# Kernel tuning notes

Hardware: AMD Instinct MI355X
Metric: run time of the kernel (lower is better)

## Reference

```python
import jax, jax.numpy as jnp
import numpy as np

DIM = 24
HID = 256
N = 4096
NUM_LO = DIM * (DIM - 1) // 2  # 276
NEG = -0.01  # slope used in the hand-written Jacobians (source uses -0.01, NOT the fwd leaky slope 0.01; faithful)


def _linear_params(key, out_dim, in_dim):
    kw, kb = jax.random.split(key)
    s = 1.0 / np.sqrt(in_dim)
    W = jax.random.uniform(kw, (out_dim, in_dim), jnp.float32, -s, s)
    b = jax.random.uniform(kb, (out_dim,), jnp.float32, -s, s)
    return W, b


def setup_inputs() -> dict:
    key = jax.random.key(0)
    k = jax.random.split(key, 7)
    W1, b1 = _linear_params(k[0], HID, DIM)
    W2, b2 = _linear_params(k[1], HID, HID)
    WG, bG = _linear_params(k[2], DIM, HID)
    WLd, bLd = _linear_params(k[3], DIM, HID)
    WLo, bLo = _linear_params(k[4], NUM_LO, HID)
    q = jax.random.normal(k[5], (N, DIM), jnp.float32)
    q_dot = jax.random.normal(k[6], (N, DIM), jnp.float32)
    return {"q": q, "q_dot": q_dot, "W1": W1, "b1": b1, "W2": W2, "b2": b2,
            "WG": WG, "bG": bG, "WLd": WLd, "bLd": bLd, "WLo": WLo, "bLo": bLo}


def _forward(q, q_dot, W1, b1, W2, b2, WG, bG, WLd, bLd, WLo, bLo):
    n, d = q.shape
    tr, tc = np.tril_indices(d, -1)  # row-major strict-lower order == torch mask-flatten order
    di = np.arange(d)
    # MLP trunk (torch leaky_relu default slope 0.01)
    h1 = jax.nn.leaky_relu(q @ W1.T + b1)                       # [n,HID]
    h2 = jax.nn.leaky_relu(h1 @ W2.T + b2)                      # [n,HID]
    h3 = h2 @ WLd.T + bLd                                       # [n,d]
    g = h2 @ WG.T + bG                                          # [n,d]
    Ld = jax.nn.softplus(h3)                                    # [n,d]
    Lo = h2 @ WLo.T + bLo                                       # [n,NUM_LO]
    # Lower-triangular L (diag_embed(Ld) + masked strict-lower fill)
    L = jnp.zeros((n, d, d), q.dtype).at[:, tr, tc].set(Lo).at[:, di, di].set(Ld)
    # Hand-written Jacobian chain; diag_embed(v)@W == v[:,:,None]*W (direct elementwise scaling)
    dR1 = jnp.where(h1 > 0, 1.0, NEG)
    J1 = dR1[:, :, None] * W1                                    # dh1/dq  [n,HID,d]
    dR2 = jnp.where(h2 > 0, 1.0, NEG)
    J2 = dR2[:, :, None] * jnp.einsum('ij,njd->nid', W2, J1)     # dh2/dq  [n,HID,d]
    sig = jax.nn.sigmoid(h3)
    dld_dq = sig[:, :, None] * jnp.einsum('ij,njd->nid', WLd, J2)  # [n,d,d]
    dlo_dq = jnp.einsum('oj,njd->nod', WLo, J2)                  # [n,NUM_LO,d]
    dld_dt = jnp.einsum('nid,nd->ni', dld_dq, q_dot)             # [n,d]
    dlo_dt = jnp.einsum('nod,nd->no', dlo_dq, q_dot)             # [n,NUM_LO]
    dL_dt = jnp.zeros((n, d, d), q.dtype).at[:, tr, tc].set(dlo_dt).at[:, di, di].set(dld_dt)
    # 4D assembly: torch does L[L==1] = dlo_dq.view(-1), which reinterprets the (lo, q_idx)
    # flat buffer in (q_idx, tril_pos) order -> plain reshape replicates that exactly.
    vals = dlo_dq.reshape(n, d, NUM_LO)
    dld_dq_p = dld_dq.transpose(0, 2, 1)                         # [n, d_q, d_ld]
    dL_dq = jnp.zeros((n, d, d, d), q.dtype).at[:, :, tr, tc].set(vals).at[:, :, di, di].set(dld_dq_p)
    eye = jnp.eye(d, dtype=q.dtype)
    M = L @ L.transpose(0, 2, 1) + 1e-9 * eye
    dM_dt = L @ dL_dt.transpose(0, 2, 1) + dL_dt @ L.transpose(0, 2, 1)
    # Quadratic term. torch: q_dot.repeat(d,1)/L.repeat(d,1,1) index as (i % n) while
    # dL_dq.view(n*d,d,d) indexes as (i // d, i % d) -> replicate exactly (faithful).
    idx = jnp.arange(n * d) % n
    qd_r = q_dot[idx]                                            # [n*d, d]
    L_r = L[idx]                                                 # [n*d, d, d]
    dL_i = dL_dq.reshape(n * d, d, d)
    S = dL_i @ L_r.transpose(0, 2, 1) + L_r @ dL_i.transpose(0, 2, 1)
    quad = jnp.einsum('bi,bij,bj->b', qd_r, S, qd_r).reshape(n, d)
    c = jnp.einsum('nij,nj->ni', dM_dt, q_dot) - 0.5 * quad
    return M, c, g


def reference(q, q_dot, W1, b1, W2, b2, WG, bG, WLd, bLd, WLo, bLo):
    return _forward(q, q_dot, W1, b1, W2, b2, WG, bG, WLd, bLd, WLo, bLo)
```

## Files before the change

### kernel.cpp

```cpp
#include <hip/hip_runtime.h>
#include <math.h>

#define DIM 24
#define HID 256
#define NLO 276
#define NSAMP 4096
#define C_OFF 2359296
#define G_OFF 2457600

#define OFF_W2FH 0
#define OFF_W2FL 32768
#define OFF_WEFH 65536
#define OFF_WEFL 106496
#define OFF_W1H16 147456
#define OFF_W1L16 151552
#define OFF_W2H16 155648
#define OFF_W2L16 188416
#define OFF_WHH16 221184
#define OFF_WHL16 264192
#define OFF_MSKT 307200
#define OFF_SIGT 372736
#define OFF_LDT  471040
#define OFF_UT   569344
#define OFF_LOT  667648

typedef __attribute__((ext_vector_type(8))) short bf16x8;
typedef __attribute__((ext_vector_type(8))) _Float16 f16x8;
typedef __attribute__((ext_vector_type(4))) float f32x4;

__device__ __forceinline__ float leaky(float x){ return x > 0.f ? x : 0.01f*x; }
__device__ __forceinline__ unsigned short f2b(float f){
  unsigned u = __float_as_uint(f);
  return (unsigned short)((u + 0x7FFFu + ((u >> 16) & 1u)) >> 16);
}
__device__ __forceinline__ float b2f(unsigned short h){ return __uint_as_float(((unsigned)h) << 16); }
__device__ __forceinline__ void f2h2(float v, unsigned short* hi, unsigned short* lo){
  _Float16 h = (_Float16)v;
  _Float16 l = (_Float16)((v - (float)h) * 4096.f);
  *hi = *(unsigned short*)&h; *lo = *(unsigned short*)&l;
}

__global__ __launch_bounds__(256) void k0_prep(
    const float* __restrict__ W1, const float* __restrict__ W2,
    const float* __restrict__ WG, const float* __restrict__ WLd,
    const float* __restrict__ WLo, float* __restrict__ ws)
{
  const int tid = blockIdx.x*256 + threadIdx.x;
  const int nth = gridDim.x*256;
  unsigned short* W2FH = (unsigned short*)(ws + OFF_W2FH);
  unsigned short* W2FL = (unsigned short*)(ws + OFF_W2FL);
  for (int e = tid; e < 65536; e += nth){
    int j=e&7, l=(e>>3)&63, kb=(e>>9)&7, mt=e>>12;
    int m = mt*16+(l&15), k = kb*32+((l>>4)&3)*8+j;
    float v = W2[m*256+k];
    unsigned short h = f2b(v);
    W2FH[e]=h; W2FL[e]=f2b(v-b2f(h));
  }
  unsigned short* WEFH = (unsigned short*)(ws + OFF_WEFH);
  unsigned short* WEFL = (unsigned short*)(ws + OFF_WEFL);
  for (int e = tid; e < 81920; e += nth){
    int j=e&7, l=(e>>3)&63, kb=(e>>9)&7, mt=e>>12;
    int r = mt*16+(l&15), k = kb*32+((l>>4)&3)*8+j;
    float v = 0.f;
    if (r < 24) v = WLd[r*256+k]; else if (r < 300) v = WLo[(r-24)*256+k];
    unsigned short h = f2b(v);
    WEFH[e]=h; WEFL[e]=f2b(v-b2f(h));
  }
  unsigned short* W1H = (unsigned short*)(ws + OFF_W1H16);
  unsigned short* W1L = (unsigned short*)(ws + OFF_W1L16);
  for (int e = tid; e < 8192; e += nth){
    int j=e&7, l=(e>>3)&63, mt=e>>9;
    int m = mt*16+(l&15), k = ((l>>4)&3)*8+j;
    float v = (k < 24) ? W1[m*24+k] : 0.f;
    f2h2(v, &W1H[e], &W1L[e]);
  }
  unsigned short* W2H = (unsigned short*)(ws + OFF_W2H16);
  unsigned short* W2L = (unsigned short*)(ws + OFF_W2L16);
  for (int e = tid; e < 65536; e += nth){
    int j=e&7, l=(e>>3)&63, kb=(e>>9)&7, mt=e>>12;
    int m = mt*16+(l&15), k = kb*32+((l>>4)&3)*8+j;
    f2h2(W2[m*256+k], &W2H[e], &W2L[e]);
  }
  unsigned short* WHH = (unsigned short*)(ws + OFF_WHH16);
  unsigned short* WHL = (unsigned short*)(ws + OFF_WHL16);
  for (int e = tid; e < 86016; e += nth){
    int j=e&7, l=(e>>3)&63, kb=(e>>9)&7, mt=e>>12;
    int rr = mt*16+(l&15), k = kb*32+((l>>4)&3)*8+j;
    float v = 0.f;
    if (rr < 24) v = WLd[rr*256+k];
    else if (rr < 48) v = WG[(rr-24)*256+k];
    else if (rr < 324) v = WLo[(rr-48)*256+k];
    f2h2(v, &WHH[e], &WHL[e]);
  }
}

__global__ __launch_bounds__(256) void k1_fwd(
    const float* __restrict__ q,
    const float* __restrict__ b1, const float* __restrict__ b2,
    const float* __restrict__ bG, const float* __restrict__ bLd,
    const float* __restrict__ bLo, float* __restrict__ ws,
    float* __restrict__ out)
{
  const int s0 = blockIdx.x*8, t = threadIdx.x;
  const int w = t>>6, l = t&63, l15 = l&15, l4g = (l>>4)&3;
  unsigned* MSKT = (unsigned*)(ws + OFF_MSKT);
  float* SIGT = ws + OFF_SIGT;
  float* LDT  = ws + OFF_LDT;
  float* LOT  = ws + OFF_LOT;

  __shared__ __align__(16) unsigned short pool[8448];
  __shared__ unsigned char mb[8][64];
  unsigned short* BQH = pool;
  unsigned short* BQL = BQH + 320;
  unsigned short* BH2 = pool;
  unsigned short* BL2 = BH2 + 2112;

  for (int f = t; f < 192; f += 256){
    float v = q[s0*24 + f];
    int n = f/24, k = f%24;
    f2h2(v, &BQH[n*40+k], &BQL[n*40+k]);
  }
  if (t < 64){ int n = t>>3, k = 24 + (t&7); BQH[n*40+k]=0; BQL[n*40+k]=0; }
  __syncthreads();

  f32x4 aH[4], aX[4];
  #pragma unroll
  for (int i=0;i<4;++i){ aH[i]=(f32x4){0,0,0,0}; aX[i]=(f32x4){0,0,0,0}; }
  {
    const f16x8* WH = (const f16x8*)(ws + OFF_W1H16);
    const f16x8* WL = (const f16x8*)(ws + OFF_W1L16);
    f16x8 Af[4], Al[4];
    #pragma unroll
    for (int i=0;i<4;++i){ int mt=w+4*i; Af[i]=WH[mt*64+l]; Al[i]=WL[mt*64+l]; }
    int off = l15*40 + l4g*8;
    f16x8 Bh = *(const f16x8*)(BQH+off), Bl = *(const f16x8*)(BQL+off);
    #pragma unroll
    for (int i=0;i<4;++i){
      aH[i]=__builtin_amdgcn_mfma_f32_16x16x32_f16(Af[i],Bh,aH[i],0,0,0);
      aX[i]=__builtin_amdgcn_mfma_f32_16x16x32_f16(Af[i],Bl,aX[i],0,0,0);
      aX[i]=__builtin_amdgcn_mfma_f32_16x16x32_f16(Al[i],Bh,aX[i],0,0,0);
    }
  }
  __syncthreads();
  #pragma unroll
  for (int i=0;i<4;++i){
    int m0=(w+4*i)*16+4*l4g;
    float4 bb = *(const float4*)(b1+m0);
    int n = l15;
    if (n < 8){
      unsigned nib=0; unsigned short hs[4], ls[4];
      #pragma unroll
      for (int r=0;r<4;++r){
        float val = aH[i][r] + aX[i][r]*(1.f/4096.f) + ((const float*)&bb)[r];
        if (val > 0.f) nib |= 1u<<r;
        f2h2(leaky(val), &hs[r], &ls[r]);
      }
      mb[n][(m0>>2)] = (unsigned char)nib;
      *(uint2*)(BH2 + n*264 + m0) = make_uint2((unsigned)hs[0]|((unsigned)hs[1]<<16),
                                               (unsigned)hs[2]|((unsigned)hs[3]<<16));
      *(uint2*)(BL2 + n*264 + m0) = make_uint2((unsigned)ls[0]|((unsigned)ls[1]<<16),
                                               (unsigned)ls[2]|((unsigned)ls[3]<<16));
    }
  }
  __syncthreads();
  if (t < 64){
    int n = t&7, w8 = t>>3; unsigned word = 0;
    #pragma unroll
    for (int b=0;b<8;++b) word |= (unsigned)(mb[n][w8*8+b] & 0xFu) << (4*b);
    MSKT[w8*NSAMP + s0+n] = word;
  }

  #pragma unroll
  for (int i=0;i<4;++i){ aH[i]=(f32x4){0,0,0,0}; aX[i]=(f32x4){0,0,0,0}; }
  {
    const f16x8* WH = (const f16x8*)(ws + OFF_W2H16);
    const f16x8* WL = (const f16x8*)(ws + OFF_W2L16);
    for (int kb=0;kb<8;++kb){
      f16x8 Af[4], Al[4];
      #pragma unroll
      for (int i=0;i<4;++i){ int mt=w+4*i; Af[i]=WH[(mt*8+kb)*64+l]; Al[i]=WL[(mt*8+kb)*64+l]; }
      int off = l15*264 + kb*32 + l4g*8;
      f16x8 Bh = *(const f16x8*)(BH2+off), Bl = *(const f16x8*)(BL2+off);
      #pragma unroll
      for (int i=0;i<4;++i){
        aH[i]=__builtin_amdgcn_mfma_f32_16x16x32_f16(Af[i],Bh,aH[i],0,0,0);
        aX[i]=__builtin_amdgcn_mfma_f32_16x16x32_f16(Af[i],Bl,aX[i],0,0,0);
        aX[i]=__builtin_amdgcn_mfma_f32_16x16x32_f16(Al[i],Bh,aX[i],0,0,0);
      }
    }
  }
  __syncthreads();
  #pragma unroll
  for (int i=0;i<4;++i){
    int m0=(w+4*i)*16+4*l4g;
    float4 bb = *(const float4*)(b2+m0);
    int n = l15;
    if (n < 8){
      unsigned nib=0; unsigned short hs[4], ls[4];
      #pragma unroll
      for (int r=0;r<4;++r){
        float val = aH[i][r] + aX[i][r]*(1.f/4096.f) + ((const float*)&bb)[r];
        if (val > 0.f) nib |= 1u<<r;
        f2h2(leaky(val), &hs[r], &ls[r]);
      }
      mb[n][(m0>>2)] = (unsigned char)nib;
      *(uint2*)(BH2 + n*264 + m0) = make_uint2((unsigned)hs[0]|((unsigned)hs[1]<<16),
                                               (unsigned)hs[2]|((unsigned)hs[3]<<16));
      *(uint2*)(BL2 + n*264 + m0) = make_uint2((unsigned)ls[0]|((unsigned)ls[1]<<16),
                                               (unsigned)ls[2]|((unsigned)ls[3]<<16));
    }
  }
  __syncthreads();
  if (t < 64){
    int n = t&7, w8 = t>>3; unsigned word = 0;
    #pragma unroll
    for (int b=0;b<8;++b) word |= (unsigned)(mb[n][w8*8+b] & 0xFu) << (4*b);
    MSKT[(8+w8)*NSAMP + s0+n] = word;
  }

  for (int pass=0; pass<2; ++pass){
    f32x4 cH[3], cX[3];
    #pragma unroll
    for (int i=0;i<3;++i){ cH[i]=(f32x4){0,0,0,0}; cX[i]=(f32x4){0,0,0,0}; }
    const f16x8* WH = (const f16x8*)(ws + OFF_WHH16);
    const f16x8* WL = (const f16x8*)(ws + OFF_WHL16);
    for (int kb=0;kb<8;++kb){
      f16x8 Af[3], Al[3];
      #pragma unroll
      for (int i=0;i<3;++i){
        int mt = w + 4*(3*pass+i);
        if (mt < 21){ Af[i]=WH[(mt*8+kb)*64+l]; Al[i]=WL[(mt*8+kb)*64+l]; }
      }
      int off = l15*264 + kb*32 + l4g*8;
      f16x8 Bh = *(const f16x8*)(BH2+off), Bl = *(const f16x8*)(BL2+off);
      #pragma unroll
      for (int i=0;i<3;++i){
        int mt = w + 4*(3*pass+i);
        if (mt < 21){
          cH[i]=__builtin_amdgcn_mfma_f32_16x16x32_f16(Af[i],Bh,cH[i],0,0,0);
          cX[i]=__builtin_amdgcn_mfma_f32_16x16x32_f16(Af[i],Bl,cX[i],0,0,0);
          cX[i]=__builtin_amdgcn_mfma_f32_16x16x32_f16(Al[i],Bh,cX[i],0,0,0);
        }
      }
    }
    #pragma unroll
    for (int i=0;i<3;++i){
      int mt = w + 4*(3*pass+i);
      if (mt >= 21) continue;
      int m0 = mt*16+4*l4g;
      int n = l15;
      if (n < 8){
        int sG = s0+n;
        #pragma unroll
        for (int r=0;r<4;++r){
          int rr = m0+r;
          float val = cH[i][r] + cX[i][r]*(1.f/4096.f);
          if (rr < 24){
            val += bLd[rr];
            SIGT[rr*NSAMP + sG] = 1.f/(1.f + expf(-val));
            LDT[rr*NSAMP + sG] = fmaxf(val,0.f) + log1pf(expf(-fabsf(val)));
          } else if (rr < 48){
            out[G_OFF + sG*24 + (rr-24)] = val + bG[rr-24];
          } else if (rr < 324){
            LOT[(rr-48)*NSAMP + sG] = val + bLo[rr-48];
          }
        }
      }
    }
  }
}

__global__ __launch_bounds__(256) void kU(
    const float* __restrict__ qd_g, const float* __restrict__ ws_c,
    float* __restrict__ UT)
{
  const int t = threadIdx.x, nb = blockIdx.x*256;
  const float* LDT = ws_c + OFF_LDT;
  const float* LOT = ws_c + OFF_LOT;
  __shared__ float qd_ss[256*25];
  for (int f = t; f < 6144; f += 256){
    int nl = f/24, r = f%24;
    qd_ss[nl*25 + r] = qd_g[nb*24 + f];
  }
  __syncthreads();
  const int n = nb + t;
  #pragma unroll
  for (int c = 0; c < 24; ++c){
    float u = qd_ss[t*25+c]*LDT[c*NSAMP + n];
    for (int r = c+1; r < 24; ++r)
      u += qd_ss[t*25+r]*LOT[(r*(r-1)/2 + c)*NSAMP + n];
    UT[c*NSAMP + n] = u;
  }
}

__global__ __launch_bounds__(256) void kM(
    const float* __restrict__ ws_c, float* __restrict__ out)
{
  const int n = blockIdx.x, t = threadIdx.x;
  const float* LDT = ws_c + OFF_LDT;
  const float* LOT = ws_c + OFF_LOT;
  __shared__ float Lp[600];
  for (int e = t; e < 600; e += 256) Lp[e] = 0.f;
  __syncthreads();
  if (t < 24) Lp[t*25 + t] = LDT[t*NSAMP + n];
  for (int p = t; p < 276; p += 256){
    int r = (int)((1.f + sqrtf(1.f + 8.f*(float)p))*0.5f);
    while (r*(r-1)/2 > p) --r;
    while ((r+1)*r/2 <= p) ++r;
    int c = p - r*(r-1)/2;
    Lp[r*25 + c] = LOT[p*NSAMP + n];
  }
  __syncthreads();
  for (int e = t; e < 576; e += 256){
    int r = e/24, c = e%24, km = min(r,c);
    float acc = (r == c) ? 1e-9f : 0.f;
    for (int k = 0; k <= km; ++k) acc += Lp[r*25+k]*Lp[c*25+k];
    out[(size_t)n*576 + e] = acc;
  }
}

__global__ __launch_bounds__(256, 3) void kDE(
    const float* __restrict__ q_dot, const float* __restrict__ W1g,
    float* __restrict__ ws, float* __restrict__ out)
{
  const int n0 = blockIdx.x*2, t = threadIdx.x;
  const int w = t >> 6, l = t & 63;
  const int l15 = l & 15, l4g = (l >> 4) & 3;
  const unsigned* MSKT = (const unsigned*)(ws + OFF_MSKT);
  const float* SIGT = ws + OFF_SIGT;
  const float* LDT  = ws + OFF_LDT;
  const float* UT   = ws + OFF_UT;
  const float* LOT  = ws + OFF_LOT;

  __shared__ __align__(16) char pool[50688];
  __shared__ unsigned msk[2][16];
  unsigned short* BH = (unsigned short*)pool;
  unsigned short* BL = BH + 12672;
  float* dlo_flat = (float*)pool;
  float* dld25    = (float*)(pool + 26496);
  float* qdm_s    = (float*)(pool + 28896);
  float* um_s     = (float*)(pool + 31296);
  float* qp2      = (float*)(pool + 33696);
  float* dtlo     = (float*)(pool + 40320);
  float* dtld     = (float*)(pool + 41424);
  float* w1s      = (float*)(pool + 41520);
  float* sigs     = (float*)(pool + 41616);
  float* qds      = (float*)(pool + 41712);
  float* uss      = (float*)(pool + 41808);

  if (t < 32) msk[t>>4][t&15] = MSKT[(t&15)*NSAMP + n0 + (t>>4)];
  __syncthreads();

  {
    float w1r[24];
    #pragma unroll
    for (int d = 0; d < 24; ++d) w1r[d] = W1g[t*24 + d];
    float dr0 = ((msk[0][t>>5] >> (t&31)) & 1u) ? 1.f : -0.01f;
    float dr1 = ((msk[1][t>>5] >> (t&31)) & 1u) ? 1.f : -0.01f;
    #pragma unroll
    for (int c = 0; c < 48; ++c){
      int s = c >= 24, d = c - 24*s;
      float f = (s ? dr1 : dr0) * w1r[d];
      unsigned short h = f2b(f);
      BH[c*264 + t] = h;
      BL[c*264 + t] = f2b(f - b2f(h));
    }
  }
  __syncthreads();

  f32x4 accD[4][3];
  #pragma unroll
  for (int i = 0; i < 4; ++i)
    #pragma unroll
    for (int nt = 0; nt < 3; ++nt) accD[i][nt] = (f32x4){0.f,0.f,0.f,0.f};
  {
    const bf16x8* AHp = (const bf16x8*)(ws + OFF_W2FH);
    const bf16x8* ALp = (const bf16x8*)(ws + OFF_W2FL);
    for (int kb = 0; kb < 8; ++kb){
      bf16x8 AH[4], AL[4], BHf[3], BLf[3];
      #pragma unroll
      for (int i = 0; i < 4; ++i){
        int mt = 4*w + i;
        AH[i] = AHp[(mt*8+kb)*64 + l];
        AL[i] = ALp[(mt*8+kb)*64 + l];
      }
      #pragma unroll
      for (int nt = 0; nt < 3; ++nt){
        int off = (nt*16 + l15)*264 + kb*32 + l4g*8;
        BHf[nt] = *(const bf16x8*)(BH + off);
        BLf[nt] = *(const bf16x8*)(BL + off);
      }
      #pragma unroll
      for (int i = 0; i < 4; ++i)
        #pragma unroll
        for (int nt = 0; nt < 3; ++nt){
          accD[i][nt] = __builtin_amdgcn_mfma_f32_16x16x32_bf16(AH[i], BHf[nt], accD[i][nt], 0, 0, 0);
          accD[i][nt] = __builtin_amdgcn_mfma_f32_16x16x32_bf16(AH[i], BLf[nt], accD[i][nt], 0, 0, 0);
          accD[i][nt] = __builtin_amdgcn_mfma_f32_16x16x32_bf16(AL[i], BHf[nt], accD[i][nt], 0, 0, 0);
        }
    }
  }
  __syncthreads();

  #pragma unroll
  for (int i = 0; i < 4; ++i){
    int mt = 4*w + i;
    int m0 = mt*16 + 4*l4g;
    int bb = m0 & 31;
    #pragma unroll
    for (int nt = 0; nt < 3; ++nt){
      int c = nt*16 + l15;
      int s = c >= 24;
      unsigned word = msk[s][8 + (mt>>1)];
      unsigned short hs[4], ls[4];
      #pragma unroll
      for (int r = 0; r < 4; ++r){
        float sc = ((word >> (bb + r)) & 1u) ? 1.f : -0.01f;
        float v = sc * accD[i][nt][r];
        hs[r] = f2b(v); ls[r] = f2b(v - b2f(hs[r]));
      }
      *(uint2*)(BH + c*264 + m0) = make_uint2((unsigned)hs[0] | ((unsigned)hs[1]<<16),
                                              (unsigned)hs[2] | ((unsigned)hs[3]<<16));
      *(uint2*)(BL + c*264 + m0) = make_uint2((unsigned)ls[0] | ((unsigned)ls[1]<<16),
                                              (unsigned)ls[2] | ((unsigned)ls[3]<<16));
    }
  }
  __syncthreads();

  f32x4 accE[5][3];
  #pragma unroll
  for (int i = 0; i < 5; ++i)
    #pragma unroll
    for (int nt = 0; nt < 3; ++nt) accE[i][nt] = (f32x4){0.f,0.f,0.f,0.f};
  {
    const bf16x8* AHp = (const bf16x8*)(ws + OFF_WEFH);
    const bf16x8* ALp = (const bf16x8*)(ws + OFF_WEFL);
    for (int kb = 0; kb < 8; ++kb){
      bf16x8 AH[5], AL[5], BHf[3], BLf[3];
      #pragma unroll
      for (int i = 0; i < 5; ++i){
        int mt = 5*w + i;
        AH[i] = AHp[(mt*8+kb)*64 + l];
        AL[i] = ALp[(mt*8+kb)*64 + l];
      }
      #pragma unroll
      for (int nt = 0; nt < 3; ++nt){
        int off = (nt*16 + l15)*264 + kb*32 + l4g*8;
        BHf[nt] = *(const bf16x8*)(BH + off);
        BLf[nt] = *(const bf16x8*)(BL + off);
      }
      #pragma unroll
      for (int i = 0; i < 5; ++i)
        #pragma unroll
        for (int nt = 0; nt < 3; ++nt){
          accE[i][nt] = __builtin_amdgcn_mfma_f32_16x16x32_bf16(AH[i], BHf[nt], accE[i][nt], 0, 0, 0);
          accE[i][nt] = __builtin_amdgcn_mfma_f32_16x16x32_bf16(AH[i], BLf[nt], accE[i][nt], 0, 0, 0);
          accE[i][nt] = __builtin_amdgcn_mfma_f32_16x16x32_bf16(AL[i], BHf[nt], accE[i][nt], 0, 0, 0);
        }
    }
  }
  __syncthreads();

  for (int s = 0; s < 2; ++s){
    const int n = n0 + s;
    #pragma unroll
    for (int i = 0; i < 5; ++i){
      int mt = 5*w + i;
      #pragma unroll
      for (int nt = 0; nt < 3; ++nt){
        int c = nt*16 + l15;
        if ((c >= 24) == (s == 1)){
          int d = c - 24*s;
          #pragma unroll
          for (int r = 0; r < 4; ++r){
            int re = mt*16 + 4*l4g + r;
            if (re < 24) dld25[re*25 + d] = accE[i][nt][r];
            else if (re < 300) dlo_flat[(re-24)*24 + d] = accE[i][nt][r];
          }
        }
      }
    }
    for (int e = t; e < 576; e += 256){
      int a_ = e/24, b_ = e%24;
      int ma = (n*24 + a_) & (NSAMP-1);
      int mb_ = (n*24 + b_) & (NSAMP-1);
      qdm_s[a_*25 + b_] = q_dot[ma*24 + b_];
      um_s[a_*25 + b_]  = UT[a_*NSAMP + mb_];
    }
    if (t < 24){
      sigs[t] = SIGT[t*NSAMP + n];
      qds[t]  = q_dot[n*24 + t];
      uss[t]  = UT[t*NSAMP + n];
    }
    __syncthreads();

    for (int k = t; k < 1656; k += 256){
      float4 v = *(const float4*)(dlo_flat + 4*k);
      int j4 = (k % 6)*4;
      qp2[k] = v.x*qds[j4] + v.y*qds[j4+1] + v.z*qds[j4+2] + v.w*qds[j4+3];
    }
    if (t < 24){
      float a = 0.f;
      #pragma unroll
      for (int d = 0; d < 24; ++d) a += dld25[t*25+d]*qds[d];
      dtld[t] = sigs[t]*a;
    }
    __syncthreads();

    for (int o = t; o < 276; o += 256){
      float a = 0.f;
      #pragma unroll
      for (int j = 0; j < 6; ++j) a += qp2[o*6+j];
      dtlo[o] = a;
    }
    __syncthreads();

    float quad_l = 0.f;
    if (t < 24){
      const int i = t;
      float y[24];
      #pragma unroll
      for (int k = 0; k < 24; ++k) y[k] = um_s[k*25 + i];
      #pragma unroll
      for (int c2 = 0; c2 < 24; ++c2)
        quad_l += y[c2]*qdm_s[i*25+c2]*sigs[c2]*dld25[c2*25+i];
      const float* vb = dlo_flat + i*276;
      float4 v4 = (float4){0,0,0,0};
      #pragma unroll
      for (int r = 1; r < 24; ++r){
        float zr = qdm_s[i*25+r];
        #pragma unroll
        for (int cc = 0; cc < r; ++cc){
          const int p = r*(r-1)/2 + cc;
          if ((p & 3) == 0) v4 = *(const float4*)(vb + p);
          float vbv = ((p&3)==0) ? v4.x : ((p&3)==1) ? v4.y : ((p&3)==2) ? v4.z : v4.w;
          quad_l += zr*y[cc]*vbv;
        }
      }
    } else if (t >= 64 && t < 88){
      int i = t - 64;
      float a = qds[i]*dtld[i];
      for (int j = i+1; j < 24; ++j) a += qds[j]*dtlo[j*(j-1)/2 + i];
      w1s[i] = a;
    }
    __syncthreads();

    if (t < 24){
      const int i = t;
      float cs = dtld[i]*uss[i] + LDT[i*NSAMP + n]*w1s[i];
      for (int k = 0; k < i; ++k){
        int p = i*(i-1)/2 + k;
        cs += LOT[p*NSAMP + n]*w1s[k] + dtlo[p]*uss[k];
      }
      out[C_OFF + n*24 + i] = cs - quad_l;
    }
    __syncthreads();
  }
}

extern "C" void kernel_launch(void* const* d_in, const int* in_sizes, int n_in,
                              void* d_out, int out_size, void* d_ws, size_t ws_size,
                              hipStream_t stream)
{
  const float* q   = (const float*)d_in[0];
  const float* qd  = (const float*)d_in[1];
  const float* W1  = (const float*)d_in[2];
  const float* b1  = (const float*)d_in[3];
  const float* W2  = (const float*)d_in[4];
  const float* b2  = (const float*)d_in[5];
  const float* WG  = (const float*)d_in[6];
  const float* bG  = (const float*)d_in[7];
  const float* WLd = (const float*)d_in[8];
  const float* bLd = (const float*)d_in[9];
  const float* WLo = (const float*)d_in[10];
  const float* bLo = (const float*)d_in[11];
  float* out = (float*)d_out;
  float* ws  = (float*)d_ws;

  k0_prep<<<256, 256, 0, stream>>>(W1, W2, WG, WLd, WLo, ws);
  k1_fwd<<<NSAMP/8, 256, 0, stream>>>(q, b1, b2, bG, bLd, bLo, ws, out);
  kU<<<NSAMP/256, 256, 0, stream>>>(qd, ws, ws + OFF_UT);
  kM<<<NSAMP, 256, 0, stream>>>(ws, out);
  kDE<<<NSAMP/2, 256, 0, stream>>>(qd, W1, ws, out);
}
```

Measured before the change: 266.3 us.

## Fuse M and U computation into forward kernel and precompute W1 bf16 splits

Result: faster. 254.4 us (-4.5%).

```diff
diff --git a/kernel.cpp b/kernel.cpp
--- a/kernel.cpp
+++ b/kernel.cpp
@@ -23,6 +23,10 @@
 #define OFF_LDT  471040
 #define OFF_UT   569344
 #define OFF_LOT  667648
+#define OFF_W1PH 1798144
+#define OFF_W1PL 1801216
+#define OFF_W1NH 1804288
+#define OFF_W1NL 1807360
 
 typedef __attribute__((ext_vector_type(8))) short bf16x8;
 typedef __attribute__((ext_vector_type(8))) _Float16 f16x8;
@@ -92,10 +96,22 @@
     else if (rr < 324) v = WLo[(rr-48)*256+k];
     f2h2(v, &WHH[e], &WHL[e]);
   }
+  unsigned short* W1PH = (unsigned short*)(ws + OFF_W1PH);
+  unsigned short* W1PL = (unsigned short*)(ws + OFF_W1PL);
+  unsigned short* W1NH = (unsigned short*)(ws + OFF_W1NH);
+  unsigned short* W1NL = (unsigned short*)(ws + OFF_W1NL);
+  for (int e = tid; e < 6144; e += nth){
+    float v = W1[e];
+    unsigned short h = f2b(v);
+    W1PH[e] = h; W1PL[e] = f2b(v - b2f(h));
+    float vn = -0.01f*v;
+    unsigned short hn = f2b(vn);
+    W1NH[e] = hn; W1NL[e] = f2b(vn - b2f(hn));
+  }
 }
 
 __global__ __launch_bounds__(256) void k1_fwd(
-    const float* __restrict__ q,
+    const float* __restrict__ q, const float* __restrict__ qd_g,
     const float* __restrict__ b1, const float* __restrict__ b2,
     const float* __restrict__ bG, const float* __restrict__ bLd,
     const float* __restrict__ bLo, float* __restrict__ ws,
@@ -106,10 +122,13 @@
   unsigned* MSKT = (unsigned*)(ws + OFF_MSKT);
   float* SIGT = ws + OFF_SIGT;
   float* LDT  = ws + OFF_LDT;
+  float* UT   = ws + OFF_UT;
   float* LOT  = ws + OFF_LOT;
 
   __shared__ __align__(16) unsigned short pool[8448];
   __shared__ unsigned char mb[8][64];
+  __shared__ float qd_s[8][24];
+  __shared__ float Lsm[8][600];
   unsigned short* BQH = pool;
   unsigned short* BQL = BQH + 320;
   unsigned short* BH2 = pool;
@@ -119,6 +138,7 @@
     float v = q[s0*24 + f];
     int n = f/24, k = f%24;
     f2h2(v, &BQH[n*40+k], &BQL[n*40+k]);
+    ((float*)qd_s)[f] = qd_g[s0*24 + f];
   }
   if (t < 64){ int n = t>>3, k = 24 + (t&7); BQH[n*40+k]=0; BQL[n*40+k]=0; }
   __syncthreads();
@@ -251,6 +271,14 @@
       int n = l15;
       if (n < 8){
         int sG = s0+n;
+        int tr = 0, tc = 0;
+        if (m0 >= 48){
+          int p = m0 - 48;
+          tr = (int)((1.f + sqrtf(1.f + 8.f*(float)p))*0.5f);
+          while (tr*(tr-1)/2 > p) --tr;
+          while ((tr+1)*tr/2 <= p) ++tr;
+          tc = p - tr*(tr-1)/2;
+        }
         #pragma unroll
         for (int r=0;r<4;++r){
           int rr = m0+r;
@@ -258,70 +286,42 @@
           if (rr < 24){
             val += bLd[rr];
             SIGT[rr*NSAMP + sG] = 1.f/(1.f + expf(-val));
-            LDT[rr*NSAMP + sG] = fmaxf(val,0.f) + log1pf(expf(-fabsf(val)));
+            float sp = fmaxf(val,0.f) + log1pf(expf(-fabsf(val)));
+            LDT[rr*NSAMP + sG] = sp;
+            Lsm[n][rr*25 + rr] = sp;
           } else if (rr < 48){
             out[G_OFF + sG*24 + (rr-24)] = val + bG[rr-24];
           } else if (rr < 324){
-            LOT[(rr-48)*NSAMP + sG] = val + bLo[rr-48];
+            float lov = val + bLo[rr-48];
+            LOT[(rr-48)*NSAMP + sG] = lov;
+            Lsm[n][tr*25 + tc] = lov;
+            if (++tc == tr){ ++tr; tc = 0; }
           }
         }
       }
     }
   }
+  __syncthreads();
+
+  for (int n2 = 0; n2 < 8; ++n2){
+    const float* Ls = Lsm[n2];
+    for (int e = t; e < 576; e += 256){
+      int r = e/24, c = e%24, km = min(r,c);
+      float acc = (r == c) ? 1e-9f : 0.f;
+      for (int k = 0; k <= km; ++k) acc += Ls[r*25+k]*Ls[c*25+k];
+      out[(size_t)(s0+n2)*576 + e] = acc;
+    }
+  }
+  if (t < 192){
+    int n = t/24, c = t%24;
+    float u = qd_s[n][c]*Lsm[n][c*25+c];
+    for (int r = c+1; r < 24; ++r) u += qd_s[n][r]*Lsm[n][r*25+c];
+    UT[c*NSAMP + s0+n] = u;
+  }
 }
 
-__global__ __launch_bounds__(256) void kU(
-    const float* __restrict__ qd_g, const float* __restrict__ ws_c,
-    float* __restrict__ UT)
-{
-  const int t = threadIdx.x, nb = blockIdx.x*256;
-  const float* LDT = ws_c + OFF_LDT;
-  const float* LOT = ws_c + OFF_LOT;
-  __shared__ float qd_ss[256*25];
-  for (int f = t; f < 6144; f += 256){
-    int nl = f/24, r = f%24;
-    qd_ss[nl*25 + r] = qd_g[nb*24 + f];
-  }
-  __syncthreads();
-  const int n = nb + t;
-  #pragma unroll
-  for (int c = 0; c < 24; ++c){
-    float u = qd_ss[t*25+c]*LDT[c*NSAMP + n];
-    for (int r = c+1; r < 24; ++r)
-      u += qd_ss[t*25+r]*LOT[(r*(r-1)/2 + c)*NSAMP + n];
-    UT[c*NSAMP + n] = u;
-  }
-}
-
-__global__ __launch_bounds__(256) void kM(
-    const float* __restrict__ ws_c, float* __restrict__ out)
-{
-  const int n = blockIdx.x, t = threadIdx.x;
-  const float* LDT = ws_c + OFF_LDT;
-  const float* LOT = ws_c + OFF_LOT;
-  __shared__ float Lp[600];
-  for (int e = t; e < 600; e += 256) Lp[e] = 0.f;
-  __syncthreads();
-  if (t < 24) Lp[t*25 + t] = LDT[t*NSAMP + n];
-  for (int p = t; p < 276; p += 256){
-    int r = (int)((1.f + sqrtf(1.f + 8.f*(float)p))*0.5f);
-    while (r*(r-1)/2 > p) --r;
-    while ((r+1)*r/2 <= p) ++r;
-    int c = p - r*(r-1)/2;
-    Lp[r*25 + c] = LOT[p*NSAMP + n];
-  }
-  __syncthreads();
-  for (int e = t; e < 576; e += 256){
-    int r = e/24, c = e%24, km = min(r,c);
-    float acc = (r == c) ? 1e-9f : 0.f;
-    for (int k = 0; k <= km; ++k) acc += Lp[r*25+k]*Lp[c*25+k];
-    out[(size_t)n*576 + e] = acc;
-  }
-}
-
 __global__ __launch_bounds__(256, 3) void kDE(
-    const float* __restrict__ q_dot, const float* __restrict__ W1g,
-    float* __restrict__ ws, float* __restrict__ out)
+    const float* __restrict__ q_dot, float* __restrict__ ws, float* __restrict__ out)
 {
   const int n0 = blockIdx.x*2, t = threadIdx.x;
   const int w = t >> 6, l = t & 63;
@@ -347,23 +347,29 @@
   float* sigs     = (float*)(pool + 41616);
   float* qds      = (float*)(pool + 41712);
   float* uss      = (float*)(pool + 41808);
+  float* qps      = (float*)(pool + 41904);
 
   if (t < 32) msk[t>>4][t&15] = MSKT[(t&15)*NSAMP + n0 + (t>>4)];
   __syncthreads();
 
   {
-    float w1r[24];
-    #pragma unroll
-    for (int d = 0; d < 24; ++d) w1r[d] = W1g[t*24 + d];
-    float dr0 = ((msk[0][t>>5] >> (t&31)) & 1u) ? 1.f : -0.01f;
-    float dr1 = ((msk[1][t>>5] >> (t&31)) & 1u) ? 1.f : -0.01f;
-    #pragma unroll
-    for (int c = 0; c < 48; ++c){
-      int s = c >= 24, d = c - 24*s;
-      float f = (s ? dr1 : dr0) * w1r[d];
-      unsigned short h = f2b(f);
-      BH[c*264 + t] = h;
-      BL[c*264 + t] = f2b(f - b2f(h));
+    bool p0 = (msk[0][t>>5] >> (t&31)) & 1u;
+    bool p1 = (msk[1][t>>5] >> (t&31)) & 1u;
+    const unsigned* h0 = (const unsigned*)((const unsigned short*)(ws + (p0 ? OFF_W1PH : OFF_W1NH)) + t*24);
+    const unsigned* l0 = (const unsigned*)((const unsigned short*)(ws + (p0 ? OFF_W1PL : OFF_W1NL)) + t*24);
+    const unsigned* h1 = (const unsigned*)((const unsigned short*)(ws + (p1 ? OFF_W1PH : OFF_W1NH)) + t*24);
+    const unsigned* l1 = (const unsigned*)((const unsigned short*)(ws + (p1 ? OFF_W1PL : OFF_W1NL)) + t*24);
+    #pragma unroll
+    for (int j = 0; j < 12; ++j){
+      unsigned dh0 = h0[j], dl0 = l0[j], dh1 = h1[j], dl1 = l1[j];
+      BH[(2*j)*264 + t]      = (unsigned short)dh0;
+      BH[(2*j+1)*264 + t]    = (unsigned short)(dh0 >> 16);
+      BL[(2*j)*264 + t]      = (unsigned short)dl0;
+      BL[(2*j+1)*264 + t]    = (unsigned short)(dl0 >> 16);
+      BH[(24+2*j)*264 + t]   = (unsigned short)dh1;
+      BH[(24+2*j+1)*264 + t] = (unsigned short)(dh1 >> 16);
+      BL[(24+2*j)*264 + t]   = (unsigned short)dl1;
+      BL[(24+2*j+1)*264 + t] = (unsigned short)(dl1 >> 16);
     }
   }
   __syncthreads();
@@ -412,17 +418,20 @@
       int c = nt*16 + l15;
       int s = c >= 24;
       unsigned word = msk[s][8 + (mt>>1)];
-      unsigned short hs[4], ls[4];
+      unsigned uh[4], ul[4];
       #pragma unroll
       for (int r = 0; r < 4; ++r){
         float sc = ((word >> (bb + r)) & 1u) ? 1.f : -0.01f;
         float v = sc * accD[i][nt][r];
-        hs[r] = f2b(v); ls[r] = f2b(v - b2f(hs[r]));
-      }
-      *(uint2*)(BH + c*264 + m0) = make_uint2((unsigned)hs[0] | ((unsigned)hs[1]<<16),
-                                              (unsigned)hs[2] | ((unsigned)hs[3]<<16));
-      *(uint2*)(BL + c*264 + m0) = make_uint2((unsigned)ls[0] | ((unsigned)ls[1]<<16),
-                                              (unsigned)ls[2] | ((unsigned)ls[3]<<16));
+        unsigned uv = __float_as_uint(v);
+        uh[r] = uv;
+        float lo = v - __uint_as_float(uv & 0xFFFF0000u);
+        ul[r] = __float_as_uint(lo);
+      }
+      *(uint2*)(BH + c*264 + m0) = make_uint2((uh[0]>>16) | (uh[1] & 0xFFFF0000u),
+                                              (uh[2]>>16) | (uh[3] & 0xFFFF0000u));
+      *(uint2*)(BL + c*264 + m0) = make_uint2((ul[0]>>16) | (ul[1] & 0xFFFF0000u),
+                                              (ul[2]>>16) | (ul[3] & 0xFFFF0000u));
     }
   }
   __syncthreads();
@@ -515,30 +524,20 @@
     }
     __syncthreads();
 
-    float quad_l = 0.f;
-    if (t < 24){
-      const int i = t;
-      float y[24];
-      #pragma unroll
-      for (int k = 0; k < 24; ++k) y[k] = um_s[k*25 + i];
-      #pragma unroll
-      for (int c2 = 0; c2 < 24; ++c2)
-        quad_l += y[c2]*qdm_s[i*25+c2]*sigs[c2]*dld25[c2*25+i];
-      const float* vb = dlo_flat + i*276;
-      float4 v4 = (float4){0,0,0,0};
-      #pragma unroll
-      for (int r = 1; r < 24; ++r){
-        float zr = qdm_s[i*25+r];
-        #pragma unroll
-        for (int cc = 0; cc < r; ++cc){
-          const int p = r*(r-1)/2 + cc;
-          if ((p & 3) == 0) v4 = *(const float4*)(vb + p);
-          float vbv = ((p&3)==0) ? v4.x : ((p&3)==1) ? v4.y : ((p&3)==2) ? v4.z : v4.w;
-          quad_l += zr*y[cc]*vbv;
-        }
-      }
-    } else if (t >= 64 && t < 88){
-      int i = t - 64;
+    if (t < 96){
+      int g = t/24, i = t%24;
+      float part = 0.f;
+      for (int c2 = g; c2 < 24; c2 += 4){
+        float v = qdm_s[i*25+c2]*sigs[c2]*dld25[c2*25+i];
+        for (int r = c2+1; r < 24; ++r){
+          int p = r*(r-1)/2 + c2;
+          v += qdm_s[i*25+r]*dlo_flat[i*276 + p];
+        }
+        part += um_s[c2*25+i]*v;
+      }
+      qps[g*24 + i] = part;
+    } else if (t >= 128 && t < 152){
+      int i = t - 128;
       float a = qds[i]*dtld[i];
       for (int j = i+1; j < 24; ++j) a += qds[j]*dtlo[j*(j-1)/2 + i];
       w1s[i] = a;
@@ -552,7 +551,8 @@
         int p = i*(i-1)/2 + k;
         cs += LOT[p*NSAMP + n]*w1s[k] + dtlo[p]*uss[k];
       }
-      out[C_OFF + n*24 + i] = cs - quad_l;
+      float quad = qps[i] + qps[24+i] + qps[48+i] + qps[72+i];
+      out[C_OFF + n*24 + i] = cs - quad;
     }
     __syncthreads();
   }
@@ -578,8 +578,6 @@
   float* ws  = (float*)d_ws;
 
   k0_prep<<<256, 256, 0, stream>>>(W1, W2, WG, WLd, WLo, ws);
-  k1_fwd<<<NSAMP/8, 256, 0, stream>>>(q, b1, b2, bG, bLd, bLo, ws, out);
-  kU<<<NSAMP/256, 256, 0, stream>>>(qd, ws, ws + OFF_UT);
-  kM<<<NSAMP, 256, 0, stream>>>(ws, out);
-  kDE<<<NSAMP/2, 256, 0, stream>>>(qd, W1, ws, out);
+  k1_fwd<<<NSAMP/8, 256, 0, stream>>>(q, qd, b1, b2, bG, bLd, bLo, ws, out);
+  kDE<<<NSAMP/2, 256, 0, stream>>>(qd, ws, out);
 }
```
